# Optimization experiments

Hardware: AMD Instinct MI355X
Metric: run time of the kernel (lower is better)

The kernel has to match this reference:

```python
import jax, jax.numpy as jnp
import numpy as np

DIM = 512
HEADS = 8
DIM_HEAD = 64
INNER = HEADS * DIM_HEAD


def setup_inputs() -> dict:
    key = jax.random.key(0)
    k1, k2, k3, k4 = jax.random.split(key, 4)
    x = jax.random.normal(k1, (4, 8192, DIM), dtype=jnp.float32)
    # nn.Linear(dim, inner*3, bias=False): weight applied as x @ W^T; store transposed form [dim, 3*inner]
    w_qkv = jax.random.normal(k2, (DIM, 3 * INNER), dtype=jnp.float32) / np.sqrt(DIM)
    w_out = jax.random.normal(k3, (INNER, DIM), dtype=jnp.float32) / np.sqrt(INNER)
    b_out = jax.random.normal(k4, (DIM,), dtype=jnp.float32) * 0.01
    return {"x": x, "w_qkv": w_qkv, "w_out": w_out, "b_out": b_out}


def reference(x, w_qkv, w_out, b_out):
    b, n, d = x.shape
    qkv = x @ w_qkv  # [b, n, 3*inner]
    q, k, v = jnp.split(qkv, 3, axis=-1)

    def to_heads(t):
        return t.reshape(b, n, HEADS, DIM_HEAD).transpose(0, 2, 1, 3)  # [b,h,n,dh]

    q, k, v = map(to_heads, (q, k, v))
    q = jax.nn.elu(q) + 1.0
    k = jax.nn.elu(k) + 1.0
    # kv summary: [b,h,dh,dh]
    kv = jnp.einsum('bhnd,bhnm->bhdm', k, v)
    # normalizer z: [b,h,n]  (note: original does NOT apply self.scale)
    z = 1.0 / (jnp.einsum('bhnd,bhd->bhn', q, k.sum(axis=2)) + 1e-6)
    out = jnp.einsum('bhnd,bhdm->bhnm', q, kv) * z[..., None]  # [b,h,n,dh]
    out = out.transpose(0, 2, 1, 3).reshape(b, n, INNER)
    return out @ w_out + b_out
```

## Files before the change

kernel.cpp:

```cpp
#include <hip/hip_runtime.h>
#include <hip/hip_bf16.h>

#define B_SZ 4
#define SEQ 8192
#define DIM 512
#define HEADS 8
#define DH 64
#define INNER 512
#define QKV_COLS 1536
#define M_TOT (B_SZ * SEQ)
#define BHN (B_SZ * HEADS)

typedef __bf16 bf16x8 __attribute__((ext_vector_type(8)));
typedef __bf16 bf16x4 __attribute__((ext_vector_type(4)));
typedef float f32x4 __attribute__((ext_vector_type(4)));

__device__ __forceinline__ float elu1(float x) {
    return x > 0.f ? x + 1.f : __expf(x);
}

__device__ __forceinline__ void gl_lds16(const void* g, void* l) {
    __builtin_amdgcn_global_load_lds(
        (const __attribute__((address_space(1))) unsigned int*)g,
        (__attribute__((address_space(3))) unsigned int*)l, 16, 0, 0);
}

#define MFMA16(a, b, c) __builtin_amdgcn_mfma_f32_16x16x32_bf16(a, b, c, 0, 0, 0)
#define BARRIER() asm volatile("s_barrier" ::: "memory")

__global__ void convert_all(const float* __restrict__ x,
                            const float* __restrict__ w_qkv,
                            const float* __restrict__ w_out,
                            __bf16* __restrict__ xb,
                            __bf16* __restrict__ wqkv_t,
                            __bf16* __restrict__ wout_t) {
    const int NX = M_TOT * DIM / 4;
    int id = blockIdx.x * 256 + threadIdx.x;
    if (id < NX) {
        float4 f = reinterpret_cast<const float4*>(x)[id];
        bf16x4 h = {(__bf16)f.x, (__bf16)f.y, (__bf16)f.z, (__bf16)f.w};
        reinterpret_cast<bf16x4*>(xb)[id] = h;
        return;
    }
    int id2 = id - NX;
    if (id2 < QKV_COLS * DIM) {
        int n = id2 / DIM, k = id2 % DIM;
        wqkv_t[id2] = (__bf16)w_qkv[k * QKV_COLS + n];
    } else {
        int id3 = id2 - QKV_COLS * DIM;
        if (id3 < INNER * DIM) {
            int n = id3 / DIM, k = id3 % DIM;
            wout_t[id3] = (__bf16)w_out[k * DIM + n];
        }
    }
}

#define TSTR 136
__launch_bounds__(256, 2)
__global__ void gemm_qkv(const __bf16* __restrict__ xb,
                         const __bf16* __restrict__ wqkv_t,
                         __bf16* __restrict__ q_ws,
                         __bf16* __restrict__ kT_ws,
                         __bf16* __restrict__ vT_ws) {
    __shared__ __attribute__((aligned(16))) char smem[128 * TSTR * 2];
    __bf16* As = (__bf16*)smem;
    __bf16* Bs = (__bf16*)(smem + 16384);
    __bf16* T  = (__bf16*)smem;

    const int tid = threadIdx.x;
    const int wid = tid >> 6;
    const int lane = tid & 63;
    const int wm = wid >> 1, wn = wid & 1;
    const int lq = lane >> 4, lr = lane & 15;
    const int m0 = blockIdx.x * 128;
    const int n0 = blockIdx.y * 128;
    const int lrow = lane >> 3;
    const int lsw  = ((lane & 7) ^ lrow) * 8;

    f32x4 acc[4][4] = {};

    for (int kb = 0; kb < DIM; kb += 64) {
#pragma unroll
        for (int t = 0; t < 4; ++t) {
            int qi = wid * 4 + t;
            int row = qi * 8 + lrow;
            gl_lds16(&xb[(size_t)(m0 + row) * DIM + kb + lsw], &As[qi * 512]);
            gl_lds16(&wqkv_t[(size_t)(n0 + row) * DIM + kb + lsw], &Bs[qi * 512]);
        }
        __syncthreads();
#pragma unroll
        for (int ks = 0; ks < 2; ++ks) {
            const int csw = ((ks * 4 + lq) ^ (lr & 7)) * 8;
            bf16x8 af[4], bfv[4];
#pragma unroll
            for (int i = 0; i < 4; ++i)
                af[i] = *reinterpret_cast<const bf16x8*>(
                    &As[(wm * 64 + i * 16 + lr) * 64 + csw]);
#pragma unroll
            for (int j = 0; j < 4; ++j)
                bfv[j] = *reinterpret_cast<const bf16x8*>(
                    &Bs[(wn * 64 + j * 16 + lr) * 64 + csw]);
#pragma unroll
            for (int i = 0; i < 4; ++i)
#pragma unroll
                for (int j = 0; j < 4; ++j)
                    acc[i][j] = MFMA16(af[i], bfv[j], acc[i][j]);
        }
        __syncthreads();
    }

    const int which = n0 / INNER;
    const int n0w = n0 % INNER;
    const int b = m0 / SEQ;
    const int nbase = m0 % SEQ;

    if (which == 0) {
#pragma unroll
        for (int i = 0; i < 4; ++i)
#pragma unroll
            for (int j = 0; j < 4; ++j) {
                int col = wn * 64 + j * 16 + lr;
#pragma unroll
                for (int r = 0; r < 4; ++r)
                    T[(wm * 64 + i * 16 + lq * 4 + r) * TSTR + col] =
                        (__bf16)elu1(acc[i][j][r]);
            }
        __syncthreads();
#pragma unroll
        for (int it = 0; it < 8; ++it) {
            int c = tid + it * 256;
            int row = c >> 4, dc = (c & 15) * 8;
            bf16x8 v = *reinterpret_cast<const bf16x8*>(&T[row * TSTR + dc]);
            int col = n0w + dc;
            int h = col >> 6, d = col & 63;
            *reinterpret_cast<bf16x8*>(
                &q_ws[(((size_t)(b * HEADS + h)) * SEQ + nbase + row) * DH + d]) = v;
        }
    } else {
        __bf16* dst = (which == 1) ? kT_ws : vT_ws;
#pragma unroll
        for (int i = 0; i < 4; ++i)
#pragma unroll
            for (int j = 0; j < 4; ++j) {
                int col = wn * 64 + j * 16 + lr;
                int rowb = wm * 64 + i * 16 + lq * 4;
                bf16x4 h4;
#pragma unroll
                for (int r = 0; r < 4; ++r) {
                    float v = acc[i][j][r];
                    h4[r] = (__bf16)((which == 1) ? elu1(v) : v);
                }
                *reinterpret_cast<bf16x4*>(&T[col * TSTR + rowb]) = h4;
            }
        __syncthreads();
#pragma unroll
        for (int it = 0; it < 8; ++it) {
            int c = tid + it * 256;
            int colIdx = c >> 4, rc = (c & 15) * 8;
            bf16x8 v = *reinterpret_cast<const bf16x8*>(&T[colIdx * TSTR + rc]);
            int gcol = n0w + colIdx;
            int h = gcol >> 6, d = gcol & 63;
            *reinterpret_cast<bf16x8*>(
                &dst[(((size_t)(b * HEADS + h)) * DH + d) * SEQ + nbase + rc]) = v;
        }
    }
}

__device__ __forceinline__ void gemm256_core(
    const __bf16* __restrict__ Am, const __bf16* __restrict__ Bm,
    int m0, int n0, char* smem, f32x4 acc[8][4])
{
    const int tid = threadIdx.x;
    const int wid = tid >> 6;
    const int lane = tid & 63;
    const int wm = wid >> 2, wn = wid & 3;
    const int lq = lane >> 4, lr = lane & 15;
    const int lrow = lane >> 3;
    const int lsw  = ((lane & 7) ^ lrow) * 8;

    __bf16* const As0 = (__bf16*)smem;
    __bf16* const Bs0 = (__bf16*)(smem + 32768);
    __bf16* const As1 = (__bf16*)(smem + 65536);
    __bf16* const Bs1 = (__bf16*)(smem + 98304);

    const int csw0 = ((0 + lq) ^ (lr & 7)) * 8;
    const int csw1 = ((4 + lq) ^ (lr & 7)) * 8;

    auto stageB = [&](__bf16* Bs, int kt, int u) {
        gl_lds16(&Bm[(size_t)(n0 + u * 64 + wid * 8 + lrow) * 512 + kt * 64 + lsw],
                 Bs + (u * 64 + wid * 8) * 64);
    };
    auto stageA = [&](__bf16* As, int kt, int s2) {
        int gr = (wid < 4) ? (s2 * 32 + wid * 8) : (128 + s2 * 32 + (wid - 4) * 8);
        gl_lds16(&Am[(size_t)(m0 + gr + lrow) * 512 + kt * 64 + lsw],
                 As + gr * 64);
    };
    auto ldA = [&](const __bf16* As, int m, int csw) -> bf16x8 {
        return *reinterpret_cast<const bf16x8*>(As + (wm * 128 + m * 16 + lr) * 64 + csw);
    };
    auto ldB = [&](const __bf16* Bs, int n, int csw) -> bf16x8 {
        return *reinterpret_cast<const bf16x8*>(Bs + (wn * 64 + n * 16 + lr) * 64 + csw);
    };

    stageB(Bs0, 0, 0); stageB(Bs0, 0, 1); stageB(Bs0, 0, 2); stageB(Bs0, 0, 3);
    stageA(As0, 0, 0); stageA(As0, 0, 1); stageA(As0, 0, 2); stageA(As0, 0, 3);
    asm volatile("s_waitcnt vmcnt(3)" ::: "memory");
    BARRIER();

#pragma unroll 2
    for (int t = 0; t < 8; ++t) {
        __bf16* const As  = (t & 1) ? As1 : As0;
        __bf16* const Bs  = (t & 1) ? Bs1 : Bs0;
        __bf16* const Asn = (t & 1) ? As0 : As1;
        __bf16* const Bsn = (t & 1) ? Bs0 : Bs1;
        const bool pf = (t < 7);
        bf16x8 bfr[4][2];

        {
            bf16x8 a00 = ldA(As, 0, csw0), a01 = ldA(As, 0, csw1);
            bf16x8 a10 = ldA(As, 1, csw0), a11 = ldA(As, 1, csw1);
#pragma unroll
            for (int n = 0; n < 4; ++n) { bfr[n][0] = ldB(Bs, n, csw0); bfr[n][1] = ldB(Bs, n, csw1); }
            if (pf) { stageB(Bsn, t + 1, 0); stageB(Bsn, t + 1, 1); }
            __builtin_amdgcn_s_setprio(1);
#pragma unroll
            for (int n = 0; n < 4; ++n) {
                acc[0][n] = MFMA16(a00, bfr[n][0], acc[0][n]);
                acc[0][n] = MFMA16(a01, bfr[n][1], acc[0][n]);
                acc[1][n] = MFMA16(a10, bfr[n][0], acc[1][n]);
                acc[1][n] = MFMA16(a11, bfr[n][1], acc[1][n]);
            }
            __builtin_amdgcn_s_setprio(0);
            if (pf) asm volatile("s_waitcnt vmcnt(4)" ::: "memory");
            else    asm volatile("s_waitcnt vmcnt(2)" ::: "memory");
            BARRIER();
        }
        {
            bf16x8 a00 = ldA(As, 2, csw0), a01 = ldA(As, 2, csw1);
            bf16x8 a10 = ldA(As, 3, csw0), a11 = ldA(As, 3, csw1);
            if (pf) { stageB(Bsn, t + 1, 2); stageB(Bsn, t + 1, 3); }
            __builtin_amdgcn_s_setprio(1);
#pragma unroll
            for (int n = 0; n < 4; ++n) {
                acc[2][n] = MFMA16(a00, bfr[n][0], acc[2][n]);
                acc[2][n] = MFMA16(a01, bfr[n][1], acc[2][n]);
                acc[3][n] = MFMA16(a10, bfr[n][0], acc[3][n]);
                acc[3][n] = MFMA16(a11, bfr[n][1], acc[3][n]);
            }
            __builtin_amdgcn_s_setprio(0);
            if (pf) asm volatile("s_waitcnt vmcnt(5)" ::: "memory");
            else    asm volatile("s_waitcnt vmcnt(1)" ::: "memory");
            BARRIER();
        }
        {
            bf16x8 a00 = ldA(As, 4, csw0), a01 = ldA(As, 4, csw1);
            bf16x8 a10 = ldA(As, 5, csw0), a11 = ldA(As, 5, csw1);
            if (pf) { stageA(Asn, t + 1, 0); stageA(Asn, t + 1, 1); }
            __builtin_amdgcn_s_setprio(1);
#pragma unroll
            for (int n = 0; n < 4; ++n) {
                acc[4][n] = MFMA16(a00, bfr[n][0], acc[4][n]);
                acc[4][n] = MFMA16(a01, bfr[n][1], acc[4][n]);
                acc[5][n] = MFMA16(a10, bfr[n][0], acc[5][n]);
                acc[5][n] = MFMA16(a11, bfr[n][1], acc[5][n]);
            }
            __builtin_amdgcn_s_setprio(0);
            if (pf) asm volatile("s_waitcnt vmcnt(6)" ::: "memory");
            else    asm volatile("s_waitcnt vmcnt(0)" ::: "memory");
            BARRIER();
        }
        {
            bf16x8 a00 = ldA(As, 6, csw0), a01 = ldA(As, 6, csw1);
            bf16x8 a10 = ldA(As, 7, csw0), a11 = ldA(As, 7, csw1);
            if (pf) { stageA(Asn, t + 1, 2); stageA(Asn, t + 1, 3); }
            __builtin_amdgcn_s_setprio(1);
#pragma unroll
            for (int n = 0; n < 4; ++n) {
                acc[6][n] = MFMA16(a00, bfr[n][0], acc[6][n]);
                acc[6][n] = MFMA16(a01, bfr[n][1], acc[6][n]);
                acc[7][n] = MFMA16(a10, bfr[n][0], acc[7][n]);
                acc[7][n] = MFMA16(a11, bfr[n][1], acc[7][n]);
            }
            __builtin_amdgcn_s_setprio(0);
            if (pf) asm volatile("s_waitcnt vmcnt(3)" ::: "memory");
            BARRIER();
        }
    }
}

__launch_bounds__(256, 2)
__global__ void kv_reduce(const __bf16* __restrict__ kT,
                          const __bf16* __restrict__ vT,
                          float* __restrict__ kv_t,
                          float* __restrict__ ksum) {
    __shared__ __attribute__((aligned(16))) __bf16 Ks[64][136];
    __shared__ __attribute__((aligned(16))) __bf16 Vs[64][136];
    const int tid = threadIdx.x;
    const int wid = tid >> 6;
    const int lane = tid & 63;
    const int lq = lane >> 4, lr = lane & 15;
    const int bh = blockIdx.y;
    const int n0 = blockIdx.x * 512;
    const size_t base = (size_t)bh * DH * SEQ;
    f32x4 acc[4] = {};
    f32x4 acc1 = {};
    bf16x8 ones8;
#pragma unroll
    for (int e = 0; e < 8; ++e) ones8[e] = (__bf16)1.f;

    for (int ch = 0; ch < 4; ++ch) {
        int nc = n0 + ch * 128;
#pragma unroll
        for (int t = 0; t < 4; ++t) {
            int c = tid + t * 256;
            int row = c >> 4, kc = (c & 15) * 8;
            *reinterpret_cast<bf16x8*>(&Ks[row][kc]) =
                *reinterpret_cast<const bf16x8*>(&kT[base + (size_t)row * SEQ + nc + kc]);
            *reinterpret_cast<bf16x8*>(&Vs[row][kc]) =
                *reinterpret_cast<const bf16x8*>(&vT[base + (size_t)row * SEQ + nc + kc]);
        }
        __syncthreads();
#pragma unroll
        for (int ks = 0; ks < 4; ++ks) {
            bf16x8 a = *reinterpret_cast<const bf16x8*>(&Ks[wid * 16 + lr][ks * 32 + lq * 8]);
            acc1 = MFMA16(a, ones8, acc1);
#pragma unroll
            for (int j = 0; j < 4; ++j) {
                bf16x8 b = *reinterpret_cast<const bf16x8*>(&Vs[j * 16 + lr][ks * 32 + lq * 8]);
                acc[j] = MFMA16(a, b, acc[j]);
            }
        }
        __syncthreads();
    }
    float* dst = kv_t + (size_t)bh * DH * DH;
#pragma unroll
    for (int j = 0; j < 4; ++j) {
        int m = j * 16 + lr;
#pragma unroll
        for (int r = 0; r < 4; ++r) {
            int d = wid * 16 + lq * 4 + r;
            atomicAdd(&dst[m * DH + d], acc[j][r]);
        }
    }
    if (lr == 0) {
#pragma unroll
        for (int r = 0; r < 4; ++r)
            atomicAdd(&ksum[bh * DH + wid * 16 + lq * 4 + r], acc1[r]);
    }
}

__launch_bounds__(256, 2)
__global__ void attn_kernel(const __bf16* __restrict__ q_ws,
                            const float* __restrict__ kv_t,
                            const float* __restrict__ ksum,
                            __bf16* __restrict__ attn) {
    __shared__ __attribute__((aligned(16))) __bf16 Qs[128][72];
    __shared__ __attribute__((aligned(16))) __bf16 KVs[64][72];
    __shared__ float zs[128];
    __shared__ float ks_s[64];
    const int tid = threadIdx.x;
    const int wid = tid >> 6, lane = tid & 63;
    const int lq = lane >> 4, lr = lane & 15;
    const int bh = blockIdx.y;
    const int b = bh >> 3, h = bh & 7;
    const int n0 = blockIdx.x * 128;
    const size_t qbase = ((size_t)bh * SEQ + n0) * DH;

#pragma unroll
    for (int t = 0; t < 4; ++t) {
        int c = tid + t * 256;
        int row = c >> 3, kc = (c & 7) * 8;
        *reinterpret_cast<bf16x8*>(&Qs[row][kc]) =
            *reinterpret_cast<const bf16x8*>(&q_ws[qbase + (size_t)row * DH + kc]);
    }
    const float* kvsrc = kv_t + (size_t)bh * DH * DH;
#pragma unroll
    for (int t = 0; t < 4; ++t) {
        int c = tid + t * 256;
        int m = c >> 4, dc = (c & 15) * 4;
        float4 f = *reinterpret_cast<const float4*>(&kvsrc[m * DH + dc]);
        bf16x4 h4 = {(__bf16)f.x, (__bf16)f.y, (__bf16)f.z, (__bf16)f.w};
        *reinterpret_cast<bf16x4*>(&KVs[m][dc]) = h4;
    }
    if (tid < 64) ks_s[tid] = ksum[bh * DH + tid];
    __syncthreads();
    {
        int row = tid >> 1, part = tid & 1;
        float s = 0.f;
#pragma unroll
        for (int j = 0; j < 32; ++j)
            s += (float)Qs[row][part * 32 + j] * ks_s[part * 32 + j];
        s += __shfl_xor(s, 1, 64);
        if (part == 0) zs[row] = 1.f / (s + 1e-6f);
    }
    __syncthreads();

    f32x4 acc[2][4] = {};
#pragma unroll
    for (int ks = 0; ks < 2; ++ks) {
        bf16x8 a0 = *reinterpret_cast<const bf16x8*>(&Qs[wid * 32 + lr][ks * 32 + lq * 8]);
        bf16x8 a1 = *reinterpret_cast<const bf16x8*>(&Qs[wid * 32 + 16 + lr][ks * 32 + lq * 8]);
#pragma unroll
        for (int j = 0; j < 4; ++j) {
            bf16x8 bfr = *reinterpret_cast<const bf16x8*>(&KVs[j * 16 + lr][ks * 32 + lq * 8]);
            acc[0][j] = MFMA16(a0, bfr, acc[0][j]);
            acc[1][j] = MFMA16(a1, bfr, acc[1][j]);
        }
    }
    __syncthreads();
#pragma unroll
    for (int mt = 0; mt < 2; ++mt)
#pragma unroll
        for (int j = 0; j < 4; ++j) {
            int m = j * 16 + lr;
#pragma unroll
            for (int r = 0; r < 4; ++r) {
                int row = wid * 32 + mt * 16 + lq * 4 + r;
                Qs[row][m] = (__bf16)(acc[mt][j][r] * zs[row]);
            }
        }
    __syncthreads();
#pragma unroll
    for (int it = 0; it < 4; ++it) {
        int c = tid + it * 256;
        int row = c >> 3, mc = (c & 7) * 8;
        bf16x8 v = *reinterpret_cast<const bf16x8*>(&Qs[row][mc]);
        *reinterpret_cast<bf16x8*>(
            &attn[((size_t)(b * SEQ + n0 + row)) * INNER + h * DH + mc]) = v;
    }
}

__launch_bounds__(512, 2)
__global__ void gemm_out(const __bf16* __restrict__ attn,
                         const __bf16* __restrict__ wout_t,
                         const float* __restrict__ b_out,
                         float* __restrict__ out) {
    __shared__ __attribute__((aligned(16))) char smem[131072];
    const int f  = blockIdx.y * gridDim.x + blockIdx.x;
    const int xc = f & 7, sl = f >> 3;
    const int m0 = (xc * 16 + (sl >> 1)) * 256;
    const int n0 = (sl & 1) * 256;

    f32x4 acc[8][4] = {};
    gemm256_core(attn, wout_t, m0, n0, smem, acc);

    const int tid = threadIdx.x;
    const int wid = tid >> 6;
    const int lane = tid & 63;
    const int wm = wid >> 2, wn = wid & 3;
    const int lq = lane >> 4, lr = lane & 15;

#pragma unroll
    for (int n = 0; n < 4; ++n) {
        int col = n0 + wn * 64 + n * 16 + lr;
        float bias = b_out[col];
#pragma unroll
        for (int m = 0; m < 8; ++m) {
            int row = m0 + wm * 128 + m * 16 + lq * 4;
#pragma unroll
            for (int r = 0; r < 4; ++r)
                out[(size_t)(row + r) * DIM + col] = acc[m][n][r] + bias;
        }
    }
}

extern "C" void kernel_launch(void* const* d_in, const int* in_sizes, int n_in,
                              void* d_out, int out_size, void* d_ws, size_t ws_size,
                              hipStream_t stream) {
    (void)in_sizes; (void)n_in; (void)out_size; (void)ws_size;
    const float* x     = (const float*)d_in[0];
    const float* w_qkv = (const float*)d_in[1];
    const float* w_out = (const float*)d_in[2];
    const float* b_out = (const float*)d_in[3];
    float* out = (float*)d_out;

    char* ws = (char*)d_ws;
    size_t off = 0;
    auto alloc = [&](size_t bytes) {
        char* p = ws + off;
        off += (bytes + 255) & ~(size_t)255;
        return p;
    };
    __bf16* xb     = (__bf16*)alloc((size_t)M_TOT * DIM * 2);
    __bf16* attn   = xb;
    __bf16* q_ws   = (__bf16*)alloc((size_t)BHN * SEQ * DH * 2);
    __bf16* kT_ws  = (__bf16*)alloc((size_t)BHN * SEQ * DH * 2);
    __bf16* vT_ws  = (__bf16*)alloc((size_t)BHN * SEQ * DH * 2);
    float*  kv_t   = (float*)alloc((size_t)BHN * DH * DH * 4 + (size_t)BHN * DH * 4);
    float*  ksum   = kv_t + (size_t)BHN * DH * DH;
    __bf16* wqkv_t = (__bf16*)alloc((size_t)QKV_COLS * DIM * 2);
    __bf16* wout_t = (__bf16*)alloc((size_t)INNER * DIM * 2);

    hipMemsetAsync(kv_t, 0, (size_t)BHN * DH * DH * 4 + (size_t)BHN * DH * 4, stream);
    convert_all<<<dim3(M_TOT * DIM / 4 / 256 + (QKV_COLS * DIM + INNER * DIM) / 256),
                  256, 0, stream>>>(x, w_qkv, w_out, xb, wqkv_t, wout_t);
    gemm_qkv<<<dim3(M_TOT / 128, QKV_COLS / 128), 256, 0, stream>>>(
        xb, wqkv_t, q_ws, kT_ws, vT_ws);
    kv_reduce<<<dim3(16, BHN), 256, 0, stream>>>(kT_ws, vT_ws, kv_t, ksum);
    attn_kernel<<<dim3(SEQ / 128, BHN), 256, 0, stream>>>(q_ws, kv_t, ksum, attn);
    gemm_out<<<dim3(M_TOT / 256, DIM / 256), 512, 0, stream>>>(attn, wout_t, b_out, out);
}
```

Baseline: 269.3 us.

## Fold kv summary into per-batch output weights and drop attention kernel

Reassociates (q·kv)·W_out as q·(kv·W_out): a small kernel builds a per-batch 512x512 weight W2 from kv and W_out, a lightweight kernel applies the z normalizer in place on q, and the output GEMM then consumes q directly with W2. Q is written row-major from the QKV GEMM instead of head-major, so the separate attention MFMA kernel and its attn buffer round trip are removed. The cost is an extra launch, writing W2, and an added bf16 rounding of the kv·W_out product.

```diff
diff --git a/kernel.cpp b/kernel.cpp
--- a/kernel.cpp
+++ b/kernel.cpp
@@ -59,7 +59,7 @@
 __launch_bounds__(256, 2)
 __global__ void gemm_qkv(const __bf16* __restrict__ xb,
                          const __bf16* __restrict__ wqkv_t,
-                         __bf16* __restrict__ q_ws,
+                         __bf16* __restrict__ qz,
                          __bf16* __restrict__ kT_ws,
                          __bf16* __restrict__ vT_ws) {
     __shared__ __attribute__((aligned(16))) char smem[128 * TSTR * 2];
@@ -131,10 +131,8 @@
             int c = tid + it * 256;
             int row = c >> 4, dc = (c & 15) * 8;
             bf16x8 v = *reinterpret_cast<const bf16x8*>(&T[row * TSTR + dc]);
-            int col = n0w + dc;
-            int h = col >> 6, d = col & 63;
             *reinterpret_cast<bf16x8*>(
-                &q_ws[(((size_t)(b * HEADS + h)) * SEQ + nbase + row) * DH + d]) = v;
+                &qz[(size_t)(m0 + row) * INNER + n0 + dc]) = v;
         }
     } else {
         __bf16* dst = (which == 1) ? kT_ws : vT_ws;
@@ -349,100 +347,100 @@
     }
 }
 
-__launch_bounds__(256, 2)
-__global__ void attn_kernel(const __bf16* __restrict__ q_ws,
-                            const float* __restrict__ kv_t,
-                            const float* __restrict__ ksum,
-                            __bf16* __restrict__ attn) {
-    __shared__ __attribute__((aligned(16))) __bf16 Qs[128][72];
-    __shared__ __attribute__((aligned(16))) __bf16 KVs[64][72];
-    __shared__ float zs[128];
-    __shared__ float ks_s[64];
+__launch_bounds__(256)
+__global__ void w2_kernel(const float* __restrict__ kv_t,
+                          const __bf16* __restrict__ wout_t,
+                          __bf16* __restrict__ W2) {
+    __shared__ __bf16 kvT[64 * 72];
     const int tid = threadIdx.x;
+    const int bh = blockIdx.x;
+    const int b = bh >> 3, h = bh & 7;
+    for (int j = tid; j < 4096; j += 256) {
+        int m = j >> 6, d = j & 63;
+        kvT[d * 72 + m] = (__bf16)kv_t[(size_t)bh * 4096 + j];
+    }
+    __syncthreads();
     const int wid = tid >> 6, lane = tid & 63;
     const int lq = lane >> 4, lr = lane & 15;
-    const int bh = blockIdx.y;
-    const int b = bh >> 3, h = bh & 7;
-    const int n0 = blockIdx.x * 128;
-    const size_t qbase = ((size_t)bh * SEQ + n0) * DH;
-
-#pragma unroll
-    for (int t = 0; t < 4; ++t) {
-        int c = tid + t * 256;
-        int row = c >> 3, kc = (c & 7) * 8;
-        *reinterpret_cast<bf16x8*>(&Qs[row][kc]) =
-            *reinterpret_cast<const bf16x8*>(&q_ws[qbase + (size_t)row * DH + kc]);
-    }
-    const float* kvsrc = kv_t + (size_t)bh * DH * DH;
-#pragma unroll
-    for (int t = 0; t < 4; ++t) {
-        int c = tid + t * 256;
-        int m = c >> 4, dc = (c & 15) * 4;
-        float4 f = *reinterpret_cast<const float4*>(&kvsrc[m * DH + dc]);
-        bf16x4 h4 = {(__bf16)f.x, (__bf16)f.y, (__bf16)f.z, (__bf16)f.w};
-        *reinterpret_cast<bf16x4*>(&KVs[m][dc]) = h4;
-    }
-    if (tid < 64) ks_s[tid] = ksum[bh * DH + tid];
+    const int c0 = wid * 128;
+    f32x4 acc[8][4] = {};
+#pragma unroll
+    for (int ks = 0; ks < 2; ++ks) {
+        bf16x8 bfv[4];
+#pragma unroll
+        for (int ni = 0; ni < 4; ++ni)
+            bfv[ni] = *reinterpret_cast<const bf16x8*>(
+                &kvT[(ni * 16 + lr) * 72 + ks * 32 + lq * 8]);
+#pragma unroll
+        for (int mi = 0; mi < 8; ++mi) {
+            bf16x8 af = *reinterpret_cast<const bf16x8*>(
+                &wout_t[(size_t)(c0 + mi * 16 + lr) * 512 + h * 64 + ks * 32 + lq * 8]);
+#pragma unroll
+            for (int ni = 0; ni < 4; ++ni)
+                acc[mi][ni] = MFMA16(af, bfv[ni], acc[mi][ni]);
+        }
+    }
+#pragma unroll
+    for (int mi = 0; mi < 8; ++mi)
+#pragma unroll
+        for (int ni = 0; ni < 4; ++ni) {
+            int d = ni * 16 + lr;
+#pragma unroll
+            for (int r = 0; r < 4; ++r) {
+                int c = c0 + mi * 16 + lq * 4 + r;
+                W2[((size_t)b * 512 + c) * 512 + h * 64 + d] = (__bf16)acc[mi][ni][r];
+            }
+        }
+}
+
+__launch_bounds__(256)
+__global__ void z_scale(__bf16* __restrict__ q,
+                        const float* __restrict__ ksum) {
+    __shared__ float ks[8][64];
+    const int tid = threadIdx.x;
+    const int m0 = blockIdx.x * 32;
+    const int b = m0 >> 13;
+    if (tid < 128) {
+        int h = tid >> 4, d4 = (tid & 15) * 4;
+        float4 f = *reinterpret_cast<const float4*>(&ksum[(b * 8 + h) * 64 + d4]);
+        ks[h][d4] = f.x; ks[h][d4 + 1] = f.y; ks[h][d4 + 2] = f.z; ks[h][d4 + 3] = f.w;
+    }
     __syncthreads();
-    {
-        int row = tid >> 1, part = tid & 1;
-        float s = 0.f;
-#pragma unroll
-        for (int j = 0; j < 32; ++j)
-            s += (float)Qs[row][part * 32 + j] * ks_s[part * 32 + j];
-        s += __shfl_xor(s, 1, 64);
-        if (part == 0) zs[row] = 1.f / (s + 1e-6f);
-    }
-    __syncthreads();
-
-    f32x4 acc[2][4] = {};
-#pragma unroll
-    for (int ks = 0; ks < 2; ++ks) {
-        bf16x8 a0 = *reinterpret_cast<const bf16x8*>(&Qs[wid * 32 + lr][ks * 32 + lq * 8]);
-        bf16x8 a1 = *reinterpret_cast<const bf16x8*>(&Qs[wid * 32 + 16 + lr][ks * 32 + lq * 8]);
-#pragma unroll
-        for (int j = 0; j < 4; ++j) {
-            bf16x8 bfr = *reinterpret_cast<const bf16x8*>(&KVs[j * 16 + lr][ks * 32 + lq * 8]);
-            acc[0][j] = MFMA16(a0, bfr, acc[0][j]);
-            acc[1][j] = MFMA16(a1, bfr, acc[1][j]);
-        }
-    }
-    __syncthreads();
-#pragma unroll
-    for (int mt = 0; mt < 2; ++mt)
-#pragma unroll
-        for (int j = 0; j < 4; ++j) {
-            int m = j * 16 + lr;
-#pragma unroll
-            for (int r = 0; r < 4; ++r) {
-                int row = wid * 32 + mt * 16 + lq * 4 + r;
-                Qs[row][m] = (__bf16)(acc[mt][j][r] * zs[row]);
-            }
-        }
-    __syncthreads();
-#pragma unroll
-    for (int it = 0; it < 4; ++it) {
-        int c = tid + it * 256;
-        int row = c >> 3, mc = (c & 7) * 8;
-        bf16x8 v = *reinterpret_cast<const bf16x8*>(&Qs[row][mc]);
-        *reinterpret_cast<bf16x8*>(
-            &attn[((size_t)(b * SEQ + n0 + row)) * INNER + h * DH + mc]) = v;
+    const int row = m0 + (tid >> 3);
+    const int h = tid & 7;
+    __bf16* p = q + (size_t)row * 512 + h * 64;
+    bf16x8 v[8];
+    float s = 0.f;
+#pragma unroll
+    for (int i = 0; i < 8; ++i) {
+        v[i] = *reinterpret_cast<const bf16x8*>(p + i * 8);
+#pragma unroll
+        for (int j = 0; j < 8; ++j) s += (float)v[i][j] * ks[h][i * 8 + j];
+    }
+    float zv = 1.f / (s + 1e-6f);
+#pragma unroll
+    for (int i = 0; i < 8; ++i) {
+        bf16x8 o;
+#pragma unroll
+        for (int j = 0; j < 8; ++j) o[j] = (__bf16)((float)v[i][j] * zv);
+        *reinterpret_cast<bf16x8*>(p + i * 8) = o;
     }
 }
 
 __launch_bounds__(512, 2)
-__global__ void gemm_out(const __bf16* __restrict__ attn,
-                         const __bf16* __restrict__ wout_t,
-                         const float* __restrict__ b_out,
-                         float* __restrict__ out) {
+__global__ void gemm_out2(const __bf16* __restrict__ qz,
+                          const __bf16* __restrict__ W2,
+                          const float* __restrict__ b_out,
+                          float* __restrict__ out) {
     __shared__ __attribute__((aligned(16))) char smem[131072];
     const int f  = blockIdx.y * gridDim.x + blockIdx.x;
     const int xc = f & 7, sl = f >> 3;
     const int m0 = (xc * 16 + (sl >> 1)) * 256;
     const int n0 = (sl & 1) * 256;
+    const int b = m0 / SEQ;
 
     f32x4 acc[8][4] = {};
-    gemm256_core(attn, wout_t, m0, n0, smem, acc);
+    gemm256_core(qz, W2 + (size_t)b * 512 * 512, m0, n0, smem, acc);
 
     const int tid = threadIdx.x;
     const int wid = tid >> 6;
@@ -482,8 +480,8 @@
         return p;
     };
     __bf16* xb     = (__bf16*)alloc((size_t)M_TOT * DIM * 2);
-    __bf16* attn   = xb;
-    __bf16* q_ws   = (__bf16*)alloc((size_t)BHN * SEQ * DH * 2);
+    __bf16* W2     = xb;
+    __bf16* qz     = (__bf16*)alloc((size_t)M_TOT * INNER * 2);
     __bf16* kT_ws  = (__bf16*)alloc((size_t)BHN * SEQ * DH * 2);
     __bf16* vT_ws  = (__bf16*)alloc((size_t)BHN * SEQ * DH * 2);
     float*  kv_t   = (float*)alloc((size_t)BHN * DH * DH * 4 + (size_t)BHN * DH * 4);
@@ -495,8 +493,9 @@
     convert_all<<<dim3(M_TOT * DIM / 4 / 256 + (QKV_COLS * DIM + INNER * DIM) / 256),
                   256, 0, stream>>>(x, w_qkv, w_out, xb, wqkv_t, wout_t);
     gemm_qkv<<<dim3(M_TOT / 128, QKV_COLS / 128), 256, 0, stream>>>(
-        xb, wqkv_t, q_ws, kT_ws, vT_ws);
+        xb, wqkv_t, qz, kT_ws, vT_ws);
     kv_reduce<<<dim3(16, BHN), 256, 0, stream>>>(kT_ws, vT_ws, kv_t, ksum);
-    attn_kernel<<<dim3(SEQ / 128, BHN), 256, 0, stream>>>(q_ws, kv_t, ksum, attn);
-    gemm_out<<<dim3(M_TOT / 256, DIM / 256), 512, 0, stream>>>(attn, wout_t, b_out, out);
-}
+    w2_kernel<<<dim3(BHN), 256, 0, stream>>>(kv_t, wout_t, W2);
+    z_scale<<<dim3(M_TOT / 32), 256, 0, stream>>>(qz, ksum);
+    gemm_out2<<<dim3(M_TOT / 256, DIM / 256), 512, 0, stream>>>(qz, W2, b_out, out);
+}
```

Measured after the change: 291.4 us. 1.08x slower.
